# Kernel optimization log

Hardware: AMD Instinct MI355X
Metric: run time of the kernel (lower is better)

The kernel has to match this reference:

```python
import jax, jax.numpy as jnp
import numpy as np

B, S, H = 2, 1024, 4096
NH, NKV, HD = 32, 8, 128
GROUPS = NH // NKV  # num_key_value_groups
ROPE_THETA = 10000.0


def setup_inputs() -> dict:
    key = jax.random.key(0)
    k0, k1, k2 = jax.random.split(key, 3)
    x = jax.random.normal(k0, (B, S, H), jnp.float32)
    w_qkv = jax.random.normal(k1, (H, (NH + 2 * NKV) * HD), jnp.float32) * (1.0 / np.sqrt(H))
    w_o = jax.random.normal(k2, (NH * HD, H), jnp.float32) * (1.0 / np.sqrt(H))
    # rotary cos/sin tables (llama freqs_cis, interleaved-pair convention)
    inv_freq = 1.0 / (ROPE_THETA ** (np.arange(0, HD, 2, dtype=np.float64) / HD))
    freqs = np.outer(np.arange(S, dtype=np.float64), inv_freq)  # [S, HD/2]
    cos = jnp.asarray(np.cos(freqs), jnp.float32)
    sin = jnp.asarray(np.sin(freqs), jnp.float32)
    # additive causal mask [1,1,S,S]
    causal = np.tril(np.ones((S, S), dtype=bool))
    mask = jnp.asarray(np.where(causal, 0.0, -1e9), jnp.float32)[None, None]
    return {"x": x, "w_qkv": w_qkv, "w_o": w_o, "cos": cos, "sin": sin, "mask": mask}


def _rope(t, cos, sin):
    # t: [B,S,N,HD]; rotate interleaved (even, odd) pairs like complex mult by freqs_cis
    t2 = t.reshape(t.shape[:-1] + (HD // 2, 2))
    t0, t1 = t2[..., 0], t2[..., 1]
    c = cos[None, :, None, :]  # [1,S,1,HD/2]
    s = sin[None, :, None, :]
    r0 = t0 * c - t1 * s
    r1 = t0 * s + t1 * c
    return jnp.stack([r0, r1], axis=-1).reshape(t.shape)


def reference(x, w_qkv, w_o, cos, sin, mask):
    b, s, _ = x.shape
    xqkv = (x @ w_qkv).reshape(b, s, NH + 2 * NKV, HD)
    xq = xqkv[:, :, :NH]                  # [b,s,NH,HD]
    xk = xqkv[:, :, NH:NH + NKV]          # [b,s,NKV,HD]
    xv = xqkv[:, :, NH + NKV:]            # [b,s,NKV,HD]
    xq = _rope(xq, cos, sin)
    xk = _rope(xk, cos, sin)
    # GQA: repeat kv heads to match query heads (repeat_interleave on head dim)
    k = jnp.repeat(xk, GROUPS, axis=2)
    v = jnp.repeat(xv, GROUPS, axis=2)
    scores = jnp.einsum('bqhd,bkhd->bhqk', xq, k) / np.float32(np.sqrt(HD))
    scores = scores + mask
    probs = jax.nn.softmax(scores.astype(jnp.float32), axis=-1).astype(xq.dtype)
    out = jnp.einsum('bhqk,bkhd->bqhd', probs, v).reshape(b, s, NH * HD)
    return out @ w_o
```

## Files before the change

kernel.cpp:

```cpp
#include <hip/hip_runtime.h>
#include <cstdint>
#include <cstddef>

typedef short bf16x8 __attribute__((ext_vector_type(8)));
typedef float f32x4 __attribute__((ext_vector_type(4)));

__device__ __forceinline__ unsigned short f2bf(float f) {
  unsigned int u = __builtin_bit_cast(unsigned int, f);
  u += 0x7fffu + ((u >> 16) & 1u);
  return (unsigned short)(u >> 16);
}

__device__ __forceinline__ void gload_lds(const unsigned short* g, unsigned short* l) {
  __builtin_amdgcn_global_load_lds(
      (const __attribute__((address_space(1))) unsigned int*)g,
      (__attribute__((address_space(3))) unsigned int*)l, 16, 0, 0);
}

__global__ void k_convert(const float* __restrict__ in, unsigned short* __restrict__ out, int n4) {
  int i = blockIdx.x * blockDim.x + threadIdx.x;
  if (i >= n4) return;
  float4 v = ((const float4*)in)[i];
  ushort4 o;
  o.x = f2bf(v.x); o.y = f2bf(v.y); o.z = f2bf(v.z); o.w = f2bf(v.w);
  ((ushort4*)out)[i] = o;
}

__global__ void k_transpose(const float* __restrict__ src, unsigned short* __restrict__ dst,
                            int K, int N) {
  __shared__ float t[32][33];
  int n0 = blockIdx.x * 32, k0 = blockIdx.y * 32;
  int tx = threadIdx.x, ty = threadIdx.y;
#pragma unroll
  for (int i = 0; i < 4; ++i)
    t[ty * 4 + i][tx] = src[(size_t)(k0 + ty * 4 + i) * N + n0 + tx];
  __syncthreads();
#pragma unroll
  for (int i = 0; i < 4; ++i)
    dst[(size_t)(n0 + ty * 4 + i) * K + k0 + tx] = f2bf(t[tx][ty * 4 + i]);
}

template <int MODE>
__global__ __launch_bounds__(256) void k_gemm(const unsigned short* __restrict__ A,
                                              const unsigned short* __restrict__ Bt,
                                              float* __restrict__ C,
                                              unsigned short* __restrict__ Qr,
                                              unsigned short* __restrict__ Kr,
                                              unsigned short* __restrict__ Vt,
                                              const float* __restrict__ cosT,
                                              const float* __restrict__ sinT,
                                              int M, int N, int K) {
  __shared__ __align__(16) unsigned short lA[128 * 64];
  __shared__ __align__(16) unsigned short lB[128 * 64];
  const int tid = threadIdx.x;
  const int lane = tid & 63, wv = tid >> 6;
  const int wr = wv >> 1, wc = wv & 1;
  const int bm = blockIdx.x * 128, bn = blockIdx.y * 128;
  const int l16 = lane & 15, lhi = lane >> 4;
  const int lrow = lane >> 3, lchunk = lane & 7;
  f32x4 acc[4][4] = {};

  const int nkt = K >> 6;
  for (int kt = 0; kt < nkt; ++kt) {
    const int k0 = kt << 6;
    __syncthreads();
#pragma unroll
    for (int j = 0; j < 4; ++j) {
      int row = wv * 32 + j * 8 + lrow;
      int sc = (lchunk ^ (row & 7)) * 8;
      gload_lds(A + (size_t)(bm + row) * K + k0 + sc, lA + (wv * 32 + j * 8) * 64);
      gload_lds(Bt + (size_t)(bn + row) * K + k0 + sc, lB + (wv * 32 + j * 8) * 64);
    }
    __syncthreads();
#pragma unroll
    for (int s = 0; s < 2; ++s) {
      bf16x8 af[4], bfr[4];
#pragma unroll
      for (int f = 0; f < 4; ++f) {
        int rowa = wr * 64 + f * 16 + l16;
        af[f] = *(const bf16x8*)(lA + rowa * 64 + (((s * 4 + lhi) ^ (rowa & 7)) * 8));
        int rowb = wc * 64 + f * 16 + l16;
        bfr[f] = *(const bf16x8*)(lB + rowb * 64 + (((s * 4 + lhi) ^ (rowb & 7)) * 8));
      }
#pragma unroll
      for (int fi = 0; fi < 4; ++fi)
#pragma unroll
        for (int fj = 0; fj < 4; ++fj)
          acc[fi][fj] = __builtin_amdgcn_mfma_f32_16x16x32_bf16(af[fi], bfr[fj], acc[fi][fj], 0, 0, 0);
    }
  }

  if (MODE == 0) {
#pragma unroll
    for (int fi = 0; fi < 4; ++fi) {
      int rbase = bm + wr * 64 + fi * 16 + lhi * 4;
#pragma unroll
      for (int fj = 0; fj < 4; ++fj) {
        int col = bn + wc * 64 + fj * 16 + l16;
#pragma unroll
        for (int r = 0; r < 4; ++r)
          C[(size_t)(rbase + r) * N + col] = acc[fi][fj][r];
      }
    }
  } else {
#pragma unroll
    for (int fi = 0; fi < 4; ++fi) {
      int rbase = bm + wr * 64 + fi * 16 + lhi * 4;
      int b = rbase >> 10, sbase = rbase & 1023;
#pragma unroll
      for (int fj = 0; fj < 4; ++fj) {
        int col = bn + wc * 64 + fj * 16 + l16;
        if (col < 5120) {
          int i = (col & 127) >> 1;
          float sgn = (col & 1) ? 1.0f : -1.0f;
          unsigned short* dst;
          if (col < 4096)
            dst = Qr + ((size_t)(b * 32 + (col >> 7)) * 1024) * 128 + (col & 127);
          else
            dst = Kr + ((size_t)(b * 8 + ((col - 4096) >> 7)) * 1024) * 128 + (col & 127);
#pragma unroll
          for (int r = 0; r < 4; ++r) {
            float own = acc[fi][fj][r];
            float other = __shfl_xor(own, 1);
            int s = sbase + r;
            float c = cosT[s * 64 + i], sn = sinT[s * 64 + i];
            dst[(size_t)s * 128] = f2bf(own * c + sgn * other * sn);
          }
        } else {
          int kvh = (col - 5120) >> 7, d = col & 127;
          unsigned short* dst = Vt + ((size_t)(b * 8 + kvh) * 128 + d) * 1024;
#pragma unroll
          for (int r = 0; r < 4; ++r) dst[sbase + r] = f2bf(acc[fi][fj][r]);
        }
      }
    }
  }
}

__global__ __launch_bounds__(256) void k_attn(const unsigned short* __restrict__ Qr,
                                              const unsigned short* __restrict__ Kr,
                                              const unsigned short* __restrict__ Vt,
                                              unsigned short* __restrict__ Out) {
  __shared__ __align__(16) unsigned short lK[64 * 128];
  __shared__ __align__(16) unsigned short lV[128 * 64];
  __shared__ __align__(16) unsigned short lP[4 * 16 * 64];
  const int tid = threadIdx.x, lane = tid & 63, wv = tid >> 6;
  const int qt = blockIdx.x, h = blockIdx.y, b = blockIdx.z;
  const int kvh = h >> 2;
  const int q0 = qt * 64;
  const int l16 = lane & 15, lhi = lane >> 4;

  const unsigned short* Qbase = Qr + ((size_t)(b * 32 + h) * 1024 + q0 + wv * 16 + l16) * 128;
  bf16x8 qf[4];
#pragma unroll
  for (int s = 0; s < 4; ++s) qf[s] = *(const bf16x8*)(Qbase + s * 32 + lhi * 8);

  const unsigned short* Kbase = Kr + (size_t)(b * 8 + kvh) * 1024 * 128;
  const unsigned short* Vbase = Vt + (size_t)(b * 8 + kvh) * 128 * 1024;

  f32x4 oacc[8] = {};
  float mrow[4] = {-1e30f, -1e30f, -1e30f, -1e30f};
  float lrow[4] = {0.f, 0.f, 0.f, 0.f};
  const int ntk = qt + 1;
  bf16x8 kreg[4], vreg[4];

#pragma unroll
  for (int i = 0; i < 4; ++i) {
    int c = tid + i * 256;
    int krow = c >> 4, kc = c & 15;
    kreg[i] = *(const bf16x8*)(Kbase + (size_t)krow * 128 + kc * 8);
    int vrow = c >> 3, vc = c & 7;
    vreg[i] = *(const bf16x8*)(Vbase + (size_t)vrow * 1024 + vc * 8);
  }

  for (int kt = 0; kt < ntk; ++kt) {
    const int k0 = kt * 64;
    __syncthreads();
#pragma unroll
    for (int i = 0; i < 4; ++i) {
      int c = tid + i * 256;
      int krow = c >> 4, kc = c & 15;
      *(bf16x8*)((char*)lK + krow * 256 + (kc ^ (krow & 7)) * 16) = kreg[i];
      int vrow = c >> 3, vc = c & 7;
      *(bf16x8*)((char*)lV + vrow * 128 + (vc ^ (vrow & 7)) * 16) = vreg[i];
    }
    __syncthreads();

    if (kt + 1 < ntk) {
      const int kn = (kt + 1) * 64;
#pragma unroll
      for (int i = 0; i < 4; ++i) {
        int c = tid + i * 256;
        int krow = c >> 4, kc = c & 15;
        kreg[i] = *(const bf16x8*)(Kbase + (size_t)(kn + krow) * 128 + kc * 8);
        int vrow = c >> 3, vc = c & 7;
        vreg[i] = *(const bf16x8*)(Vbase + (size_t)vrow * 1024 + kn + vc * 8);
      }
    }

    f32x4 sacc[4] = {};
#pragma unroll
    for (int kf = 0; kf < 4; ++kf) {
      int rowk = kf * 16 + l16;
#pragma unroll
      for (int s = 0; s < 4; ++s) {
        int ck = (s * 4 + lhi) ^ (rowk & 7);
        bf16x8 kfr = *(const bf16x8*)((char*)lK + rowk * 256 + ck * 16);
        sacc[kf] = __builtin_amdgcn_mfma_f32_16x16x32_bf16(qf[s], kfr, sacc[kf], 0, 0, 0);
      }
    }

    const int qg = q0 + wv * 16 + lhi * 4;
    float mt[4] = {-1e30f, -1e30f, -1e30f, -1e30f};
#pragma unroll
    for (int kf = 0; kf < 4; ++kf) {
      int kg = k0 + kf * 16 + l16;
#pragma unroll
      for (int r = 0; r < 4; ++r) {
        float v = sacc[kf][r] * 0.08838834764831845f;
        v = (kg <= qg + r) ? v : -1e9f;
        sacc[kf][r] = v;
        mt[r] = fmaxf(mt[r], v);
      }
    }
#pragma unroll
    for (int r = 0; r < 4; ++r) {
#pragma unroll
      for (int off = 1; off < 16; off <<= 1) mt[r] = fmaxf(mt[r], __shfl_xor(mt[r], off));
    }
    float alpha[4], rs[4];
#pragma unroll
    for (int r = 0; r < 4; ++r) {
      float mn = fmaxf(mrow[r], mt[r]);
      alpha[r] = __expf(mrow[r] - mn);
      mrow[r] = mn;
      rs[r] = 0.f;
    }
#pragma unroll
    for (int kf = 0; kf < 4; ++kf) {
      int key = kf * 16 + l16;
#pragma unroll
      for (int r = 0; r < 4; ++r) {
        float p = __expf(sacc[kf][r] - mrow[r]);
        rs[r] += p;
        int prow = lhi * 4 + r;
        int addr = wv * 2048 + ((prow * 128 + key * 2) ^ ((prow & 7) << 4));
        *(unsigned short*)((char*)lP + addr) = f2bf(p);
      }
    }
#pragma unroll
    for (int r = 0; r < 4; ++r) {
#pragma unroll
      for (int off = 1; off < 16; off <<= 1) rs[r] += __shfl_xor(rs[r], off);
      lrow[r] = lrow[r] * alpha[r] + rs[r];
    }
#pragma unroll
    for (int nf = 0; nf < 8; ++nf)
#pragma unroll
      for (int r = 0; r < 4; ++r) oacc[nf][r] *= alpha[r];

#pragma unroll
    for (int s2 = 0; s2 < 2; ++s2) {
      int prow = l16;
      int paddr = wv * 2048 + ((prow * 128 + s2 * 64 + lhi * 16) ^ ((prow & 7) << 4));
      bf16x8 pa = *(const bf16x8*)((char*)lP + paddr);
#pragma unroll
      for (int nf = 0; nf < 8; ++nf) {
        int rowd = nf * 16 + l16;
        int cv = (s2 * 4 + lhi) ^ (rowd & 7);
        bf16x8 vfr = *(const bf16x8*)((char*)lV + rowd * 128 + cv * 16);
        oacc[nf] = __builtin_amdgcn_mfma_f32_16x16x32_bf16(pa, vfr, oacc[nf], 0, 0, 0);
      }
    }
  }

  unsigned short* Ob = Out + ((size_t)(b * 1024) + q0 + wv * 16 + lhi * 4) * 4096 + h * 128;
#pragma unroll
  for (int r = 0; r < 4; ++r) {
    float inv = 1.f / lrow[r];
#pragma unroll
    for (int nf = 0; nf < 8; ++nf)
      Ob[(size_t)r * 4096 + nf * 16 + l16] = f2bf(oacc[nf][r] * inv);
  }
}

extern "C" void kernel_launch(void* const* d_in, const int* in_sizes, int n_in,
                              void* d_out, int out_size, void* d_ws, size_t ws_size,
                              hipStream_t stream) {
  const float* x = (const float*)d_in[0];
  const float* w_qkv = (const float*)d_in[1];
  const float* w_o = (const float*)d_in[2];
  const float* cosT = (const float*)d_in[3];
  const float* sinT = (const float*)d_in[4];

  char* ws = (char*)d_ws;
  unsigned short* wqkv_t = (unsigned short*)(ws);
  unsigned short* wo_t   = (unsigned short*)(ws + 50331648);
  unsigned short* xb     = (unsigned short*)(ws + 83886080);
  unsigned short* Qr     = (unsigned short*)(ws + 100663296);
  unsigned short* Kr     = (unsigned short*)(ws + 117440512);
  unsigned short* Vt     = (unsigned short*)(ws + 121634816);
  unsigned short* attn   = (unsigned short*)(ws + 125829120);

  k_convert<<<8192, 256, 0, stream>>>(x, xb, 2048 * 4096 / 4);
  k_transpose<<<dim3(6144 / 32, 4096 / 32), dim3(32, 8), 0, stream>>>(w_qkv, wqkv_t, 4096, 6144);
  k_transpose<<<dim3(4096 / 32, 4096 / 32), dim3(32, 8), 0, stream>>>(w_o, wo_t, 4096, 4096);
  k_gemm<1><<<dim3(16, 48), 256, 0, stream>>>(xb, wqkv_t, nullptr, Qr, Kr, Vt, cosT, sinT,
                                              2048, 6144, 4096);
  k_attn<<<dim3(16, 32, 2), 256, 0, stream>>>(Qr, Kr, Vt, attn);
  k_gemm<0><<<dim3(16, 32), 256, 0, stream>>>(attn, wo_t, (float*)d_out, nullptr, nullptr, nullptr,
                                              nullptr, nullptr, 2048, 4096, 4096);
}
```

Before: 390.8 us.

## Replace direct global-to-LDS loads with register-staged prefetch of next K tile

The GEMM main loop no longer uses global_load_lds to fill shared memory. Each thread now loads the next 64-wide K tile into registers while the MFMA work on the current tile runs, then writes those registers into swizzled LDS at the start of the next iteration. The aim is to hide global-memory latency behind compute with a software pipeline. In exchange it uses more VGPRs per thread and adds explicit LDS store instructions, which may lower occupancy.

```diff
diff --git a/kernel.cpp b/kernel.cpp
--- a/kernel.cpp
+++ b/kernel.cpp
@@ -9,12 +9,6 @@
   unsigned int u = __builtin_bit_cast(unsigned int, f);
   u += 0x7fffu + ((u >> 16) & 1u);
   return (unsigned short)(u >> 16);
-}
-
-__device__ __forceinline__ void gload_lds(const unsigned short* g, unsigned short* l) {
-  __builtin_amdgcn_global_load_lds(
-      (const __attribute__((address_space(1))) unsigned int*)g,
-      (__attribute__((address_space(3))) unsigned int*)l, 16, 0, 0);
 }
 
 __global__ void k_convert(const float* __restrict__ in, unsigned short* __restrict__ out, int n4) {
@@ -57,30 +51,46 @@
   const int wr = wv >> 1, wc = wv & 1;
   const int bm = blockIdx.x * 128, bn = blockIdx.y * 128;
   const int l16 = lane & 15, lhi = lane >> 4;
-  const int lrow = lane >> 3, lchunk = lane & 7;
   f32x4 acc[4][4] = {};
-
+  bf16x8 ar[4], br[4];
+
+#pragma unroll
+  for (int i = 0; i < 4; ++i) {
+    int c = tid + i * 256, row = c >> 3, c16 = c & 7;
+    ar[i] = *(const bf16x8*)(A + (size_t)(bm + row) * K + 0 + c16 * 8);
+    br[i] = *(const bf16x8*)(Bt + (size_t)(bn + row) * K + 0 + c16 * 8);
+  }
   const int nkt = K >> 6;
   for (int kt = 0; kt < nkt; ++kt) {
-    const int k0 = kt << 6;
     __syncthreads();
 #pragma unroll
-    for (int j = 0; j < 4; ++j) {
-      int row = wv * 32 + j * 8 + lrow;
-      int sc = (lchunk ^ (row & 7)) * 8;
-      gload_lds(A + (size_t)(bm + row) * K + k0 + sc, lA + (wv * 32 + j * 8) * 64);
-      gload_lds(Bt + (size_t)(bn + row) * K + k0 + sc, lB + (wv * 32 + j * 8) * 64);
+    for (int i = 0; i < 4; ++i) {
+      int c = tid + i * 256, row = c >> 3, c16 = c & 7;
+      int pc = c16 ^ (row & 7);
+      *(bf16x8*)((char*)lA + row * 128 + pc * 16) = ar[i];
+      *(bf16x8*)((char*)lB + row * 128 + pc * 16) = br[i];
     }
     __syncthreads();
+    if (kt + 1 < nkt) {
+      int kofs = (kt + 1) << 6;
+#pragma unroll
+      for (int i = 0; i < 4; ++i) {
+        int c = tid + i * 256, row = c >> 3, c16 = c & 7;
+        ar[i] = *(const bf16x8*)(A + (size_t)(bm + row) * K + kofs + c16 * 8);
+        br[i] = *(const bf16x8*)(Bt + (size_t)(bn + row) * K + kofs + c16 * 8);
+      }
+    }
 #pragma unroll
     for (int s = 0; s < 2; ++s) {
       bf16x8 af[4], bfr[4];
 #pragma unroll
       for (int f = 0; f < 4; ++f) {
         int rowa = wr * 64 + f * 16 + l16;
-        af[f] = *(const bf16x8*)(lA + rowa * 64 + (((s * 4 + lhi) ^ (rowa & 7)) * 8));
+        int ca = (s * 4 + lhi) ^ (rowa & 7);
+        af[f] = *(const bf16x8*)((char*)lA + rowa * 128 + ca * 16);
         int rowb = wc * 64 + f * 16 + l16;
-        bfr[f] = *(const bf16x8*)(lB + rowb * 64 + (((s * 4 + lhi) ^ (rowb & 7)) * 8));
+        int cb = (s * 4 + lhi) ^ (rowb & 7);
+        bfr[f] = *(const bf16x8*)((char*)lB + rowb * 128 + cb * 16);
       }
 #pragma unroll
       for (int fi = 0; fi < 4; ++fi)
```

After: 332.7 us. 14.9% less time.
